# Kernel optimization log

Measured on AMD Instinct MI355X. Metric: run time of the kernel, lower is better.

Reference implementation:

```python
import jax, jax.numpy as jnp
import numpy as np

LOG2 = float(np.log(2.0))

def ssp(x):
    # shifted softplus: ln(0.5*exp(x) + 0.5) = softplus(x) - ln(2)
    return jax.nn.softplus(x) - LOG2

N, A, F, R, E = 50000, 128, 128, 20, 1600000

def setup_inputs() -> dict:
    key = jax.random.key(0)
    ks = jax.random.split(key, 14)
    s = lambda fan_in: 1.0 / np.sqrt(fan_in)
    return {
        "x": jax.random.normal(ks[0], (N, A), dtype=jnp.float32),
        "f_ij": jax.random.uniform(ks[1], (E, R), dtype=jnp.float32),
        "rcut_ij": jax.random.uniform(ks[2], (E,), dtype=jnp.float32),
        "idx_i": jnp.sort(jax.random.randint(ks[3], (E,), 0, N)),
        "idx_j": jax.random.randint(ks[4], (E,), 0, N),
        # in2f: Dense(A -> F), no bias
        "W_in2f": jax.random.uniform(ks[5], (A, F), minval=-s(A), maxval=s(A), dtype=jnp.float32),
        # filter_network: Dense(R->F, ssp) then Dense(F->F)
        "W_f1": jax.random.uniform(ks[6], (R, F), minval=-s(R), maxval=s(R), dtype=jnp.float32),
        "b_f1": jnp.zeros((F,), dtype=jnp.float32),
        "W_f2": jax.random.uniform(ks[7], (F, F), minval=-s(F), maxval=s(F), dtype=jnp.float32),
        "b_f2": jnp.zeros((F,), dtype=jnp.float32),
        # f2out: Dense(F->A, ssp) then Dense(A->A)
        "W_o1": jax.random.uniform(ks[8], (F, A), minval=-s(F), maxval=s(F), dtype=jnp.float32),
        "b_o1": jnp.zeros((A,), dtype=jnp.float32),
        "W_o2": jax.random.uniform(ks[9], (A, A), minval=-s(A), maxval=s(A), dtype=jnp.float32),
        "b_o2": jnp.zeros((A,), dtype=jnp.float32),
    }

def reference(x, f_ij, rcut_ij, idx_i, idx_j,
              W_in2f, W_f1, b_f1, W_f2, b_f2, W_o1, b_o1, W_o2, b_o2):
    n_atoms = x.shape[0]
    # in2f projection (no bias): [N, A] -> [N, F]
    h = x @ W_in2f
    # filter MLP on edge RBF features: [E, R] -> [E, F]
    Wij = ssp(f_ij @ W_f1 + b_f1) @ W_f2 + b_f2
    Wij = Wij * rcut_ij[:, None]
    # gather neighbor features, modulate by filter, scatter-add to centers
    x_ij = h[idx_j] * Wij                                   # [E, F]
    agg = jax.ops.segment_sum(x_ij, idx_i, num_segments=n_atoms)  # [N, F]
    # f2out MLP: [N, F] -> [N, A]
    out = ssp(agg @ W_o1 + b_o1) @ W_o2 + b_o2
    return out
```

## Files before the change

kernel.cpp:

```cpp
#include <hip/hip_runtime.h>
#include <math.h>

#define LN2F 0.6931471805599453f
#define LOG2EF 1.4426950408889634f

typedef _Float16 half_t;
typedef _Float16 half4_t __attribute__((ext_vector_type(4)));
typedef _Float16 half8_t __attribute__((ext_vector_type(8)));
typedef __fp16 fp16x2 __attribute__((ext_vector_type(2)));
typedef __fp16 fp16x4 __attribute__((ext_vector_type(4)));
typedef __fp16 fp16x8 __attribute__((ext_vector_type(8)));
typedef float f32x4 __attribute__((ext_vector_type(4)));

__device__ __forceinline__ float sspf(float z) {
    return fmaxf(z, 0.f) + __logf(1.f + __expf(-fabsf(z))) - LN2F;
}
__device__ __forceinline__ half4_t cvt4(float x, float y, float z, float w) {
    half4_t r; r[0]=(half_t)x; r[1]=(half_t)y; r[2]=(half_t)z; r[3]=(half_t)w; return r;
}
__device__ __forceinline__ half8_t pk8(float a, float b, float c, float d,
                                       float e, float f, float g, float h) {
    fp16x2 p0 = __builtin_amdgcn_cvt_pkrtz(a, b);
    fp16x2 p1 = __builtin_amdgcn_cvt_pkrtz(c, d);
    fp16x2 p2 = __builtin_amdgcn_cvt_pkrtz(e, f);
    fp16x2 p3 = __builtin_amdgcn_cvt_pkrtz(g, h);
    fp16x4 lo = __builtin_shufflevector(p0, p1, 0, 1, 2, 3);
    fp16x4 hi = __builtin_shufflevector(p2, p3, 0, 1, 2, 3);
    fp16x8 v  = __builtin_shufflevector(lo, hi, 0, 1, 2, 3, 4, 5, 6, 7);
    return __builtin_bit_cast(half8_t, v);
}

__device__ __forceinline__ void load_lds16(const void* g, void* l) {
    __builtin_amdgcn_global_load_lds(
        (const __attribute__((address_space(1))) unsigned int*)g,
        (__attribute__((address_space(3))) unsigned int*)l, 16, 0, 0);
}

__device__ __forceinline__ int lbound(const int* __restrict__ a, int n, int key) {
    int lo = 0, hi = n;
    while (lo < hi) { int m = (lo + hi) >> 1; if (a[m] < key) lo = m + 1; else hi = m; }
    return lo;
}

__global__ __launch_bounds__(256) void prep_weights(
    const float* __restrict__ W_in2f, const float* __restrict__ W_f1,
    const float* __restrict__ W_f2, const float* __restrict__ W_o1,
    const float* __restrict__ W_o2,
    const float* __restrict__ b_f1, const float* __restrict__ b_f2,
    half_t* __restrict__ Wt_in2f, half_t* __restrict__ Wt_f1,
    half_t* __restrict__ W2L, half_t* __restrict__ Wt_o1,
    half_t* __restrict__ Wt_o2, float* __restrict__ b1sc, float* __restrict__ b2a)
{
    int b = blockIdx.x;
    if (b < 64) {
        int i = b*256 + threadIdx.x;
        Wt_in2f[i] = (half_t)W_in2f[(i & 127)*128 + (i >> 7)];
    } else if (b < 80) {
        int i = (b-64)*256 + threadIdx.x;
        int n = i >> 5, k = i & 31;
        Wt_f1[i] = (k < 20) ? (half_t)W_f1[k*128 + n] : (half_t)0.f;
    } else if (b < 144) {
        int i = (b-80)*256 + threadIdx.x;
        int j = i & 7, ln = (i >> 3) & 15, g = (i >> 7) & 3;
        int nt = (i >> 9) & 7, t = i >> 12;
        int k = 32*t + ((j < 4) ? (g*4 + j) : (16 + g*4 + (j - 4)));
        W2L[i] = (half_t)(LN2F * W_f2[k*128 + ln*8 + nt]);
    } else if (b < 208) {
        int i = (b-144)*256 + threadIdx.x;
        Wt_o1[i] = (half_t)W_o1[(i & 127)*128 + (i >> 7)];
    } else if (b < 272) {
        int i = (b-208)*256 + threadIdx.x;
        Wt_o2[i] = (half_t)W_o2[(i & 127)*128 + (i >> 7)];
    } else {
        int c = threadIdx.x;
        if (c < 128) {
            float s = 0.f;
            for (int k = 0; k < 128; ++k) s += W_f2[k*128 + c];
            b2a[c]  = b_f2[c] - LN2F * s;
            b1sc[c] = b_f1[c] * LOG2EF;
        }
    }
}

__global__ __launch_bounds__(256) void seg_starts(
    const int* __restrict__ idx_i, int* __restrict__ atom_start, int E, int N)
{
    int e = blockIdx.x * 256 + threadIdx.x;
    if (e >= E) return;
    int a = idx_i[e];
    int prev = (e == 0) ? -1 : idx_i[e - 1];
    for (int k = prev + 1; k <= a; ++k) atom_start[k] = e;
    if (e == E - 1)
        for (int k = a + 1; k <= N; ++k) atom_start[k] = E;
}

__global__ __launch_bounds__(256) void mfma_gemm_h(
    const float* __restrict__ A, const half_t* __restrict__ Bt,
    half_t* __restrict__ Ch, int nrows)
{
    const int tid = threadIdx.x;
    const int w = tid >> 6, l = tid & 63, g = l >> 4, ln = l & 15;
    const int r0 = blockIdx.x * 64;

    f32x4 acc[4][2];
    #pragma unroll
    for (int rf = 0; rf < 4; ++rf)
        #pragma unroll
        for (int cf = 0; cf < 2; ++cf) acc[rf][cf] = (f32x4)0.f;

    #pragma unroll
    for (int kk = 0; kk < 8; ++kk) {
        const int kb = kk * 16 + g * 4;
        half4_t a[4];
        #pragma unroll
        for (int rf = 0; rf < 4; ++rf) {
            int r = r0 + rf * 16 + ln;
            int rr = r < nrows ? r : nrows - 1;
            float4 av = *(const float4*)(A + (size_t)rr * 128 + kb);
            a[rf] = cvt4(av.x, av.y, av.z, av.w);
        }
        #pragma unroll
        for (int cf = 0; cf < 2; ++cf) {
            int n = w * 32 + cf * 16 + ln;
            half4_t b = *(const half4_t*)(Bt + (size_t)n * 128 + kb);
            #pragma unroll
            for (int rf = 0; rf < 4; ++rf)
                acc[rf][cf] = __builtin_amdgcn_mfma_f32_16x16x16f16(a[rf], b, acc[rf][cf], 0, 0, 0);
        }
    }
    #pragma unroll
    for (int cf = 0; cf < 2; ++cf) {
        int n = w * 32 + cf * 16 + ln;
        #pragma unroll
        for (int rf = 0; rf < 4; ++rf)
            #pragma unroll
            for (int reg = 0; reg < 4; ++reg) {
                int r = r0 + rf * 16 + g * 4 + reg;
                if (r < nrows) Ch[(size_t)r * 128 + n] = (half_t)acc[rf][cf][reg];
            }
    }
}

__global__ __launch_bounds__(256) void mfma_gemm2(
    const float* __restrict__ A, const half_t* __restrict__ Bt1,
    const float* __restrict__ bias1, const half_t* __restrict__ Bt2,
    const float* __restrict__ bias2, float* __restrict__ out, int nrows)
{
    __shared__ half_t ts[64][136];
    const int tid = threadIdx.x;
    const int w = tid >> 6, l = tid & 63, g = l >> 4, ln = l & 15;
    const int r0 = blockIdx.x * 64;

    f32x4 acc[4][2];
    #pragma unroll
    for (int rf = 0; rf < 4; ++rf)
        #pragma unroll
        for (int cf = 0; cf < 2; ++cf) acc[rf][cf] = (f32x4)0.f;
    #pragma unroll
    for (int kk = 0; kk < 8; ++kk) {
        const int kb = kk * 16 + g * 4;
        half4_t a[4];
        #pragma unroll
        for (int rf = 0; rf < 4; ++rf) {
            int r = r0 + rf * 16 + ln;
            int rr = r < nrows ? r : nrows - 1;
            float4 av = *(const float4*)(A + (size_t)rr * 128 + kb);
            a[rf] = cvt4(av.x, av.y, av.z, av.w);
        }
        #pragma unroll
        for (int cf = 0; cf < 2; ++cf) {
            int n = w * 32 + cf * 16 + ln;
            half4_t b = *(const half4_t*)(Bt1 + (size_t)n * 128 + kb);
            #pragma unroll
            for (int rf = 0; rf < 4; ++rf)
                acc[rf][cf] = __builtin_amdgcn_mfma_f32_16x16x16f16(a[rf], b, acc[rf][cf], 0, 0, 0);
        }
    }
    #pragma unroll
    for (int cf = 0; cf < 2; ++cf) {
        int n = w * 32 + cf * 16 + ln;
        float bv = bias1[n];
        #pragma unroll
        for (int rf = 0; rf < 4; ++rf)
            #pragma unroll
            for (int reg = 0; reg < 4; ++reg)
                ts[rf*16 + g*4 + reg][n] = (half_t)sspf(acc[rf][cf][reg] + bv);
    }
    __syncthreads();

    f32x4 acc2[4][2];
    #pragma unroll
    for (int rf = 0; rf < 4; ++rf)
        #pragma unroll
        for (int cf = 0; cf < 2; ++cf) acc2[rf][cf] = (f32x4)0.f;
    #pragma unroll
    for (int kk = 0; kk < 8; ++kk) {
        const int kb = kk * 16 + g * 4;
        half4_t a[4];
        #pragma unroll
        for (int rf = 0; rf < 4; ++rf)
            a[rf] = *(const half4_t*)&ts[rf*16 + ln][kb];
        #pragma unroll
        for (int cf = 0; cf < 2; ++cf) {
            int n = w * 32 + cf * 16 + ln;
            half4_t b = *(const half4_t*)(Bt2 + (size_t)n * 128 + kb);
            #pragma unroll
            for (int rf = 0; rf < 4; ++rf)
                acc2[rf][cf] = __builtin_amdgcn_mfma_f32_16x16x16f16(a[rf], b, acc2[rf][cf], 0, 0, 0);
        }
    }
    #pragma unroll
    for (int cf = 0; cf < 2; ++cf) {
        int n = w * 32 + cf * 16 + ln;
        float bv = bias2[n];
        #pragma unroll
        for (int rf = 0; rf < 4; ++rf)
            #pragma unroll
            for (int reg = 0; reg < 4; ++reg) {
                int r = r0 + rf * 16 + g * 4 + reg;
                if (r < nrows) out[(size_t)r * 128 + n] = acc2[rf][cf][reg] + bv;
            }
    }
}

__global__ __launch_bounds__(256, 2) void edge_kernel(
    const float* __restrict__ f_ij, const float* __restrict__ rcut,
    const int* __restrict__ idx_j,
    const half_t* __restrict__ Wt_f1, const float* __restrict__ b1sc,
    const half_t* __restrict__ W2L, const float* __restrict__ b2a,
    const half_t* __restrict__ hh, float* __restrict__ agg,
    const int* __restrict__ atom_start, int E, int N, int W)
{
    __shared__ __align__(16) half_t W2s[16384];
    __shared__ __align__(16) half_t hsh[4][2][2048];
    __shared__ float b1s[128];

    const int tid = threadIdx.x;
    const int w = tid >> 6, l = tid & 63, g = l >> 4, ln = l & 15;

    for (int i = tid; i < 2048; i += 256)
        ((float4*)W2s)[i] = ((const float4*)W2L)[i];
    if (tid < 128) b1s[tid] = b1sc[tid];
    __syncthreads();

    const int kg = blockIdx.x * 4 + w;
    const int aLo = lbound(atom_start, N + 1, (int)((size_t)kg * E / W));
    const int aHi = (kg == W - 1) ? N
                  : lbound(atom_start, N + 1, (int)((size_t)(kg + 1) * E / W));
    if (aLo >= aHi) return;

    half8_t w1f[8];
    #pragma unroll
    for (int rf = 0; rf < 8; ++rf) {
        half4_t lo = *(const half4_t*)(Wt_f1 + (size_t)(rf*16 + ln)*32 + g*4);
        half4_t hi = *(const half4_t*)(Wt_f1 + (size_t)(rf*16 + ln)*32 + 16 + g*4);
        w1f[rf] = __builtin_shufflevector(lo, hi, 0, 1, 2, 3, 4, 5, 6, 7);
    }

    f32x4 b2acc[8];
    {
        float4 blo4 = *(const float4*)(b2a + ln*8);
        float4 bhi4 = *(const float4*)(b2a + ln*8 + 4);
        float bv[8] = {blo4.x, blo4.y, blo4.z, blo4.w, bhi4.x, bhi4.y, bhi4.z, bhi4.w};
        #pragma unroll
        for (int q = 0; q < 8; ++q) {
            f32x4 t = {bv[q], bv[q], bv[q], bv[q]};
            b2acc[q] = t;
        }
    }

    int acur = aLo;
    int ends0 = atom_start[acur + 1];
    int ends1 = atom_start[min(acur + 2, N)];
    int ends2 = atom_start[min(acur + 3, N)];
    int cs = atom_start[acur];
    int ce = min(cs + 16, ends0);
    bool fl0 = (ce == ends0);
    int csn = ce;
    int cen = min(csn + 16, fl0 ? ends1 : ends0);

    int jvN[4];
    {
        int jv0[4];
        #pragma unroll
        for (int it = 0; it < 4; ++it)
            jv0[it] = idx_j[min(cs + 4*it + g, E - 1)];
        asm volatile("" ::: "memory");
        #pragma unroll
        for (int it = 0; it < 4; ++it)
            load_lds16(hh + (size_t)jv0[it]*128 + ((ln ^ it) << 3),
                       &hsh[w][0][it*512]);
        asm volatile("" ::: "memory");
    }
    float4 fA, fB;
    {
        int e = min(cs + ln, E - 1);
        fA = *(const float4*)(f_ij + (size_t)e*20 + g*4);
        fB = *(const float4*)(f_ij + (size_t)e*20 + 16);
    }
    float rc[4];
    #pragma unroll
    for (int r2 = 0; r2 < 4; ++r2) rc[r2] = rcut[min(cs + 4*g + r2, E - 1)];
    #pragma unroll
    for (int it = 0; it < 4; ++it) jvN[it] = idx_j[min(csn + 4*it + g, E - 1)];
    asm volatile("" ::: "memory");

    float racc[8];
    #pragma unroll
    for (int q = 0; q < 8; ++q) racc[q] = 0.f;
    int p = 0;

    while (acur < aHi) {
        asm volatile("" ::: "memory");
        #pragma unroll
        for (int it = 0; it < 4; ++it)
            load_lds16(hh + (size_t)jvN[it]*128 + ((ln ^ it) << 3),
                       &hsh[w][p^1][it*512]);
        asm volatile("s_waitcnt vmcnt(4)" ::: "memory");
        __builtin_amdgcn_sched_barrier(0);

        half4_t blo = cvt4(fA.x, fA.y, fA.z, fA.w);
        half4_t bhi;
        if (g == 0) bhi = cvt4(fB.x, fB.y, fB.z, fB.w);
        else { half4_t zz = {}; bhi = zz; }
        half8_t bf = __builtin_shufflevector(blo, bhi, 0, 1, 2, 3, 4, 5, 6, 7);
        float rcm[4];
        #pragma unroll
        for (int r2 = 0; r2 < 4; ++r2)
            rcm[r2] = (cs + 4*g + r2 < ce) ? rc[r2] : 0.f;
        const bool flushF = (ce == ends0);
        const bool f1 = (cen == (flushF ? ends1 : ends0));
        const int cs2 = cen;
        const int endsel = flushF ? (f1 ? ends2 : ends1) : (f1 ? ends1 : ends0);
        const int ce2 = min(cs2 + 16, endsel);

        int jv2[4];
        #pragma unroll
        for (int it = 0; it < 4; ++it)
            jv2[it] = idx_j[min(cs2 + 4*it + g, E - 1)];
        float4 fA1, fB1;
        {
            int e = min(csn + ln, E - 1);
            fA1 = *(const float4*)(f_ij + (size_t)e*20 + g*4);
            fB1 = *(const float4*)(f_ij + (size_t)e*20 + 16);
        }
        float rc1[4];
        #pragma unroll
        for (int r2 = 0; r2 < 4; ++r2) rc1[r2] = rcut[min(csn + 4*g + r2, E - 1)];
        const int aeL = atom_start[min(acur + 4, N)];
        asm volatile("" ::: "memory");

        f32x4 z[8];
        #pragma unroll
        for (int rf = 0; rf < 8; ++rf)
            z[rf] = __builtin_amdgcn_mfma_f32_16x16x32_f16(w1f[rf], bf, (f32x4)0.f, 0, 0, 0);
        half8_t a2[4];
        #pragma unroll
        for (int t = 0; t < 4; ++t) {
            float4 bbA = *(const float4*)&b1s[(2*t)*16 + g*4];
            float4 bbB = *(const float4*)&b1s[(2*t+1)*16 + g*4];
            float l0 = __log2f(1.f + exp2f(fmaf(z[2*t][0],   LOG2EF, bbA.x)));
            float l1 = __log2f(1.f + exp2f(fmaf(z[2*t][1],   LOG2EF, bbA.y)));
            float l2 = __log2f(1.f + exp2f(fmaf(z[2*t][2],   LOG2EF, bbA.z)));
            float l3 = __log2f(1.f + exp2f(fmaf(z[2*t][3],   LOG2EF, bbA.w)));
            float l4 = __log2f(1.f + exp2f(fmaf(z[2*t+1][0], LOG2EF, bbB.x)));
            float l5 = __log2f(1.f + exp2f(fmaf(z[2*t+1][1], LOG2EF, bbB.y)));
            float l6 = __log2f(1.f + exp2f(fmaf(z[2*t+1][2], LOG2EF, bbB.z)));
            float l7 = __log2f(1.f + exp2f(fmaf(z[2*t+1][3], LOG2EF, bbB.w)));
            a2[t] = pk8(l0, l1, l2, l3, l4, l5, l6, l7);
        }

        f32x4 acc[8];
        #pragma unroll
        for (int q = 0; q < 8; ++q) acc[q] = b2acc[q];
        __builtin_amdgcn_s_setprio(1);
        #pragma unroll
        for (int t = 0; t < 4; ++t)
            #pragma unroll
            for (int q = 0; q < 8; ++q) {
                half8_t bw = *(const half8_t*)&W2s[(((t*8 + q)*4 + g)*16 + ln)*8];
                acc[q] = __builtin_amdgcn_mfma_f32_16x16x32_f16(a2[t], bw, acc[q], 0, 0, 0);
            }
        __builtin_amdgcn_s_setprio(0);

        #pragma unroll
        for (int r2 = 0; r2 < 4; ++r2) {
            half8_t hv8 = *(const half8_t*)&hsh[w][p][(4*g + r2)*128 + ((ln ^ g) << 3)];
            float rr = rcm[r2];
            #pragma unroll
            for (int q = 0; q < 8; ++q)
                racc[q] = fmaf(acc[q][r2] * rr, (float)hv8[q], racc[q]);
        }

        if (flushF) {
            #pragma unroll
            for (int q = 0; q < 8; ++q) {
                float r = racc[q];
                r += __shfl_xor(r, 16, 64);
                r += __shfl_xor(r, 32, 64);
                racc[q] = r;
            }
            if (g == 0) {
                float4 v0 = {racc[0], racc[1], racc[2], racc[3]};
                float4 v1 = {racc[4], racc[5], racc[6], racc[7]};
                *(float4*)(agg + (size_t)acur*128 + ln*8)     = v0;
                *(float4*)(agg + (size_t)acur*128 + ln*8 + 4) = v1;
            }
            #pragma unroll
            for (int q = 0; q < 8; ++q) racc[q] = 0.f;
            ++acur;
            ends0 = ends1; ends1 = ends2; ends2 = aeL;
        }

        cs = csn; ce = cen; csn = cs2; cen = ce2;
        #pragma unroll
        for (int it = 0; it < 4; ++it) jvN[it] = jv2[it];
        fA = fA1; fB = fB1;
        #pragma unroll
        for (int r2 = 0; r2 < 4; ++r2) rc[r2] = rc1[r2];
        p ^= 1;
    }
}

extern "C" void kernel_launch(void* const* d_in, const int* in_sizes, int n_in,
                              void* d_out, int out_size, void* d_ws, size_t ws_size,
                              hipStream_t stream)
{
    const float* x      = (const float*)d_in[0];
    const float* f_ij   = (const float*)d_in[1];
    const float* rcut   = (const float*)d_in[2];
    const int*   idx_i  = (const int*)d_in[3];
    const int*   idx_j  = (const int*)d_in[4];
    const float* W_in2f = (const float*)d_in[5];
    const float* W_f1   = (const float*)d_in[6];
    const float* b_f1   = (const float*)d_in[7];
    const float* W_f2   = (const float*)d_in[8];
    const float* b_f2   = (const float*)d_in[9];
    const float* W_o1   = (const float*)d_in[10];
    const float* b_o1   = (const float*)d_in[11];
    const float* W_o2   = (const float*)d_in[12];
    const float* b_o2   = (const float*)d_in[13];

    const int N = in_sizes[0] / 128;
    const int E = in_sizes[2];

    half_t* h16  = (half_t*)d_ws;
    half_t* wt   = (half_t*)((char*)d_ws + (size_t)N * 128 * 4);
    half_t* Wt_in2f = wt;
    half_t* Wt_f1   = wt + 16384;
    half_t* W2L     = wt + 16384 + 4096;
    half_t* Wt_o1   = W2L + 16384;
    half_t* Wt_o2   = Wt_o1 + 16384;
    float*  b1sc    = (float*)(Wt_o2 + 16384);
    float*  b2a     = b1sc + 128;
    int* atom_start = (int*)(b2a + 128);

    prep_weights<<<273, 256, 0, stream>>>(W_in2f, W_f1, W_f2, W_o1, W_o2,
                                          b_f1, b_f2,
                                          Wt_in2f, Wt_f1, W2L, Wt_o1, Wt_o2,
                                          b1sc, b2a);
    seg_starts<<<(E + 255) / 256, 256, 0, stream>>>(idx_i, atom_start, E, N);

    const int gn  = (N + 63) / 64;
    const int nbl = 512;
    const int W   = nbl * 4;

    mfma_gemm_h<<<gn, 256, 0, stream>>>(x, Wt_in2f, h16, N);

    edge_kernel<<<nbl, 256, 0, stream>>>(f_ij, rcut, idx_j,
                                         Wt_f1, b1sc, W2L, b2a,
                                         h16, (float*)d_out, atom_start, E, N, W);

    mfma_gemm2<<<gn, 256, 0, stream>>>((const float*)d_out, Wt_o1, b_o1,
                                       Wt_o2, b_o2, (float*)d_out, N);
}
```

Before: 261.0 us.

## Replace LDS double-buffered neighbor gather with direct register prefetch in edge kernel

```diff
diff --git a/kernel.cpp b/kernel.cpp
--- a/kernel.cpp
+++ b/kernel.cpp
@@ -28,12 +28,6 @@
     fp16x4 hi = __builtin_shufflevector(p2, p3, 0, 1, 2, 3);
     fp16x8 v  = __builtin_shufflevector(lo, hi, 0, 1, 2, 3, 4, 5, 6, 7);
     return __builtin_bit_cast(half8_t, v);
-}
-
-__device__ __forceinline__ void load_lds16(const void* g, void* l) {
-    __builtin_amdgcn_global_load_lds(
-        (const __attribute__((address_space(1))) unsigned int*)g,
-        (__attribute__((address_space(3))) unsigned int*)l, 16, 0, 0);
 }
 
 __device__ __forceinline__ int lbound(const int* __restrict__ a, int n, int key) {
@@ -223,7 +217,7 @@
     }
 }
 
-__global__ __launch_bounds__(256, 2) void edge_kernel(
+__global__ __launch_bounds__(256, 4) void edge_kernel(
     const float* __restrict__ f_ij, const float* __restrict__ rcut,
     const int* __restrict__ idx_j,
     const half_t* __restrict__ Wt_f1, const float* __restrict__ b1sc,
@@ -232,7 +226,6 @@
     const int* __restrict__ atom_start, int E, int N, int W)
 {
     __shared__ __align__(16) half_t W2s[16384];
-    __shared__ __align__(16) half_t hsh[4][2][2048];
     __shared__ float b1s[128];
 
     const int tid = threadIdx.x;
@@ -274,50 +267,34 @@
     int ends1 = atom_start[min(acur + 2, N)];
     int ends2 = atom_start[min(acur + 3, N)];
     int cs = atom_start[acur];
-    int ce = min(cs + 16, ends0);
-    bool fl0 = (ce == ends0);
-    int csn = ce;
-    int cen = min(csn + 16, fl0 ? ends1 : ends0);
-
-    int jvN[4];
-    {
-        int jv0[4];
-        #pragma unroll
-        for (int it = 0; it < 4; ++it)
-            jv0[it] = idx_j[min(cs + 4*it + g, E - 1)];
-        asm volatile("" ::: "memory");
-        #pragma unroll
-        for (int it = 0; it < 4; ++it)
-            load_lds16(hh + (size_t)jv0[it]*128 + ((ln ^ it) << 3),
-                       &hsh[w][0][it*512]);
-        asm volatile("" ::: "memory");
-    }
-    float4 fA, fB;
+
+    int jv[4]; float4 fA, fB; float rc[4];
+    #pragma unroll
+    for (int r2 = 0; r2 < 4; ++r2)
+        jv[r2] = idx_j[min(cs + 4*g + r2, E - 1)];
     {
         int e = min(cs + ln, E - 1);
         fA = *(const float4*)(f_ij + (size_t)e*20 + g*4);
         fB = *(const float4*)(f_ij + (size_t)e*20 + 16);
     }
-    float rc[4];
     #pragma unroll
     for (int r2 = 0; r2 < 4; ++r2) rc[r2] = rcut[min(cs + 4*g + r2, E - 1)];
-    #pragma unroll
-    for (int it = 0; it < 4; ++it) jvN[it] = idx_j[min(csn + 4*it + g, E - 1)];
     asm volatile("" ::: "memory");
 
     float racc[8];
     #pragma unroll
     for (int q = 0; q < 8; ++q) racc[q] = 0.f;
-    int p = 0;
 
     while (acur < aHi) {
+        const int ce = min(cs + 16, ends0);
+        const int csn = ce;
+        const bool flushF = (ce == ends0);
+
+        float4 hpre[4];
+        #pragma unroll
+        for (int r2 = 0; r2 < 4; ++r2)
+            hpre[r2] = *(const float4*)(hh + (size_t)jv[r2]*128 + ln*8);
         asm volatile("" ::: "memory");
-        #pragma unroll
-        for (int it = 0; it < 4; ++it)
-            load_lds16(hh + (size_t)jvN[it]*128 + ((ln ^ it) << 3),
-                       &hsh[w][p^1][it*512]);
-        asm volatile("s_waitcnt vmcnt(4)" ::: "memory");
-        __builtin_amdgcn_sched_barrier(0);
 
         half4_t blo = cvt4(fA.x, fA.y, fA.z, fA.w);
         half4_t bhi;
@@ -328,16 +305,11 @@
         #pragma unroll
         for (int r2 = 0; r2 < 4; ++r2)
             rcm[r2] = (cs + 4*g + r2 < ce) ? rc[r2] : 0.f;
-        const bool flushF = (ce == ends0);
-        const bool f1 = (cen == (flushF ? ends1 : ends0));
-        const int cs2 = cen;
-        const int endsel = flushF ? (f1 ? ends2 : ends1) : (f1 ? ends1 : ends0);
-        const int ce2 = min(cs2 + 16, endsel);
-
-        int jv2[4];
-        #pragma unroll
-        for (int it = 0; it < 4; ++it)
-            jv2[it] = idx_j[min(cs2 + 4*it + g, E - 1)];
+
+        int jvn[4];
+        #pragma unroll
+        for (int r2 = 0; r2 < 4; ++r2)
+            jvn[r2] = idx_j[min(csn + 4*g + r2, E - 1)];
         float4 fA1, fB1;
         {
             int e = min(csn + ln, E - 1);
@@ -383,9 +355,12 @@
             }
         __builtin_amdgcn_s_setprio(0);
 
+        asm volatile("s_waitcnt vmcnt(4)" ::: "memory");
+        __builtin_amdgcn_sched_barrier(0);
+
         #pragma unroll
         for (int r2 = 0; r2 < 4; ++r2) {
-            half8_t hv8 = *(const half8_t*)&hsh[w][p][(4*g + r2)*128 + ((ln ^ g) << 3)];
+            half8_t hv8 = __builtin_bit_cast(half8_t, hpre[r2]);
             float rr = rcm[r2];
             #pragma unroll
             for (int q = 0; q < 8; ++q)
@@ -412,13 +387,10 @@
             ends0 = ends1; ends1 = ends2; ends2 = aeL;
         }
 
-        cs = csn; ce = cen; csn = cs2; cen = ce2;
-        #pragma unroll
-        for (int it = 0; it < 4; ++it) jvN[it] = jv2[it];
+        cs = csn;
+        #pragma unroll
+        for (int r2 = 0; r2 < 4; ++r2) { jv[r2] = jvn[r2]; rc[r2] = rc1[r2]; }
         fA = fA1; fB = fB1;
-        #pragma unroll
-        for (int r2 = 0; r2 < 4; ++r2) rc[r2] = rc1[r2];
-        p ^= 1;
     }
 }
 
@@ -462,7 +434,7 @@
     seg_starts<<<(E + 255) / 256, 256, 0, stream>>>(idx_i, atom_start, E, N);
 
     const int gn  = (N + 63) / 64;
-    const int nbl = 512;
+    const int nbl = 1024;
     const int W   = nbl * 4;
 
     mfma_gemm_h<<<gn, 256, 0, stream>>>(x, Wt_in2f, h16, N);
```

After: 472.1 us. 80.8% more time.
